# Kernel optimization log

Measured on AMD Instinct MI355X. Metric: run time of the kernel, lower is better.

Reference implementation:

```python
import jax, jax.numpy as jnp
import numpy as np

N_CELLS = 50000
DEG = 32
NNZ = N_CELLS * DEG
D_IN = 64
D_OUT = 64
NEG_SLOPE = 0.2


def setup_inputs() -> dict:
    key = jax.random.key(0)
    k0, k1, k2, k3, k4 = jax.random.split(key, 5)
    x_source = jax.random.normal(k0, (N_CELLS, D_IN), jnp.float32)
    # COO indices of the sparse neighborhood matrix N: DEG entries per row
    edge_rows = jnp.repeat(jnp.arange(N_CELLS, dtype=jnp.int32), DEG)
    edge_cols = jax.random.randint(k1, (NNZ,), 0, N_CELLS, dtype=jnp.int32)
    neighborhood_values = jax.random.uniform(k2, (NNZ,), jnp.float32)
    # xavier_uniform-ish scales (exact init irrelevant for correctness baseline)
    W0 = jax.random.normal(k3, (D_IN, D_OUT), jnp.float32) * (1.414 / np.sqrt(D_IN))
    a0 = jax.random.normal(k4, (2 * D_OUT, 1), jnp.float32) * 0.1
    return {
        "x_source": x_source,
        "edge_rows": edge_rows,
        "edge_cols": edge_cols,
        "neighborhood_values": neighborhood_values,
        "W0": W0,
        "a0": a0,
    }


def reference(x_source, edge_rows, edge_cols, neighborhood_values, W0, a0):
    # message = X W_p  : [n_cells, d_out]
    message = x_source @ W0
    d = message.shape[1]
    # [X_i || X_j] a  ==  (X_i a_src) + (X_j a_dst); compute node-level dot first,
    # then gather per edge (avoids materializing [nnz, 2d] concat)
    a_src = a0[:d, 0]
    a_dst = a0[d:, 0]
    node_src = message @ a_src  # [n_cells]
    node_dst = message @ a_dst  # [n_cells]
    e = jax.nn.leaky_relu(node_src[edge_rows] + node_dst[edge_cols],
                          negative_slope=NEG_SLOPE)  # [nnz]
    # sparse_row_norm: divide each edge value by its row sum (softmax=False path)
    row_sum = jax.ops.segment_sum(e, edge_rows, num_segments=N_CELLS)
    att = e / row_sum[edge_rows]
    # Hadamard product N^1 \odot A_1, then SpMM with message
    vals = neighborhood_values * att  # [nnz]
    out = jax.ops.segment_sum(vals[:, None] * message[edge_cols], edge_rows,
                              num_segments=N_CELLS)  # [n_cells, d_out]
    # update_func='relu'
    return jax.nn.relu(out)
```

## Files before the change

kernel.cpp:

```cpp
#include <hip/hip_runtime.h>
#include <hip/hip_fp16.h>

#define N_CELLS 50000
#define DEG 32
#define DIM 64
#define NEG_SLOPE 0.2

__global__ __launch_bounds__(256)
void gat_prep(const float* __restrict__ x,
              const float* __restrict__ W0,
              const float* __restrict__ a0,
              __half* __restrict__ x2,
              double* __restrict__ ns,
              double* __restrict__ nd) {
  __shared__ double2 p_s[DIM];

  const int tid = threadIdx.x;
  if (tid < DIM) {
    double ps = 0.0, pd = 0.0;
    const float4* w4 = (const float4*)(W0 + tid * DIM);
#pragma unroll
    for (int q = 0; q < DIM / 4; ++q) {
      float4 w = w4[q];
      ps = fma((double)w.x, (double)a0[4 * q + 0], ps);
      ps = fma((double)w.y, (double)a0[4 * q + 1], ps);
      ps = fma((double)w.z, (double)a0[4 * q + 2], ps);
      ps = fma((double)w.w, (double)a0[4 * q + 3], ps);
      pd = fma((double)w.x, (double)a0[DIM + 4 * q + 0], pd);
      pd = fma((double)w.y, (double)a0[DIM + 4 * q + 1], pd);
      pd = fma((double)w.z, (double)a0[DIM + 4 * q + 2], pd);
      pd = fma((double)w.w, (double)a0[DIM + 4 * q + 3], pd);
    }
    p_s[tid] = make_double2(ps, pd);
  }
  __syncthreads();

  const int gtid = blockIdx.x * 256 + tid;
  const int nthreads = gridDim.x * 256;

  const float2* xf2 = (const float2*)x;
  __half2* xh2 = (__half2*)x2;
  for (int i = gtid; i < N_CELLS * DIM / 2; i += nthreads) {
    float2 v = xf2[i];
    xh2[i] = __float22half2_rn(v);
  }

  for (int r = gtid; r < N_CELLS; r += nthreads) {
    const float4* x4 = (const float4*)(x + (size_t)r * DIM);
    double s0 = 0.0, s1 = 0.0, d0 = 0.0, d1 = 0.0;
#pragma unroll
    for (int q = 0; q < DIM / 4; ++q) {
      float4 v = x4[q];
      double2 p0 = p_s[4 * q + 0], p1 = p_s[4 * q + 1];
      double2 p2 = p_s[4 * q + 2], p3 = p_s[4 * q + 3];
      s0 = fma((double)v.x, p0.x, s0); d0 = fma((double)v.x, p0.y, d0);
      s1 = fma((double)v.y, p1.x, s1); d1 = fma((double)v.y, p1.y, d1);
      s0 = fma((double)v.z, p2.x, s0); d0 = fma((double)v.z, p2.y, d0);
      s1 = fma((double)v.w, p3.x, s1); d1 = fma((double)v.w, p3.y, d1);
    }
    ns[r] = s0 + s1;
    nd[r] = d0 + d1;
  }
}

__global__ __launch_bounds__(256)
void gat_edges(const __half* __restrict__ x2,
               const int* __restrict__ ecol,
               const float* __restrict__ nv,
               const float* __restrict__ W0,
               const double* __restrict__ ns,
               const double* __restrict__ nd,
               float* __restrict__ out) {
  __shared__ __align__(16) float w_s[4][2][DEG];
  __shared__ __align__(16) int c_s[4][2][DEG];
  __shared__ __align__(16) float h_s[4][2][DIM];

  const int lane = threadIdx.x & 63;
  const int wid = threadIdx.x >> 6;
  const int half = lane >> 5;
  const int sub = lane & 31;

  float w0c[DIM];
#pragma unroll
  for (int k = 0; k < DIM; ++k) w0c[k] = W0[k * DIM + lane];

  const int gwave = blockIdx.x * 4 + wid;
  const int nwaves = gridDim.x * 4;
  const int npairs = N_CELLS / 2;

  for (int p = gwave; p < npairs; p += nwaves) {
    const int r0 = 2 * p;
    const int myrow = r0 + half;

    const int eidx = r0 * DEG + lane;
    const int col = ecol[eidx];
    const float nvv = nv[eidx];
    double z = ns[myrow] + nd[col];
    double e = (z >= 0.0) ? z : NEG_SLOPE * z;
    double rs = e;
#pragma unroll
    for (int m = 16; m >= 1; m >>= 1) rs += __shfl_xor(rs, m, 64);
    w_s[wid][half][sub] = (float)((double)nvv * (e / rs));
    c_s[wid][half][sub] = col;

    const unsigned* xp = (const unsigned*)x2;
    float ax = 0.0f, ay = 0.0f;
#pragma unroll
    for (int j = 0; j < DEG; ++j) {
      int c = c_s[wid][half][j];
      float w = w_s[wid][half][j];
      unsigned pk = xp[(size_t)c * (DIM / 2) + sub];
      float2 xv = __half22float2(*(const __half2*)&pk);
      ax = fmaf(w, xv.x, ax);
      ay = fmaf(w, xv.y, ay);
    }
    ((float2*)h_s[wid][half])[sub] = make_float2(ax, ay);

    float oA = 0.0f, oB = 0.0f;
    const float4* hA = (const float4*)h_s[wid][0];
    const float4* hB = (const float4*)h_s[wid][1];
#pragma unroll
    for (int q = 0; q < DIM / 4; ++q) {
      float4 a = hA[q];
      float4 b = hB[q];
      oA = fmaf(a.x, w0c[4 * q + 0], oA); oB = fmaf(b.x, w0c[4 * q + 0], oB);
      oA = fmaf(a.y, w0c[4 * q + 1], oA); oB = fmaf(b.y, w0c[4 * q + 1], oB);
      oA = fmaf(a.z, w0c[4 * q + 2], oA); oB = fmaf(b.z, w0c[4 * q + 2], oB);
      oA = fmaf(a.w, w0c[4 * q + 3], oA); oB = fmaf(b.w, w0c[4 * q + 3], oB);
    }
    out[(size_t)r0 * DIM + lane] = fmaxf(oA, 0.0f);
    out[(size_t)(r0 + 1) * DIM + lane] = fmaxf(oB, 0.0f);
  }
}

extern "C" void kernel_launch(void* const* d_in, const int* in_sizes, int n_in,
                              void* d_out, int out_size, void* d_ws, size_t ws_size,
                              hipStream_t stream) {
  const float* x = (const float*)d_in[0];
  const int* ecol = (const int*)d_in[2];
  const float* nv = (const float*)d_in[3];
  const float* W0 = (const float*)d_in[4];
  const float* a0 = (const float*)d_in[5];
  float* out = (float*)d_out;

  __half* x2 = (__half*)d_ws;
  double* ns = (double*)((char*)d_ws + (size_t)N_CELLS * DIM * sizeof(__half));
  double* nd = ns + N_CELLS;

  hipLaunchKernelGGL(gat_prep, dim3(512), dim3(256), 0, stream,
                     x, W0, a0, x2, ns, nd);
  hipLaunchKernelGGL(gat_edges, dim3(2500), dim3(256), 0, stream,
                     x2, ecol, nv, W0, ns, nd, out);
}
```

Measured before the change: 127.5 us.

## Split gather into two feature-half passes with precomputed fp16 edge weights

Edge attention weights are now computed once by a separate kernel and stored as fp16, and the x fp16 copy is split into two 32-wide feature halves. The gather/projection runs in two passes, each touching only half the features so the gathered working set (3.2 MB per half) fits in cache better. The first pass writes a partial output and the second adds it and applies relu. The cost is two extra kernel launches, re-reading the column indices, an extra partial-output round trip, and fp16 rounding of the weights.

```diff
diff --git a/kernel.cpp b/kernel.cpp
--- a/kernel.cpp
+++ b/kernel.cpp
@@ -4,13 +4,16 @@
 #define N_CELLS 50000
 #define DEG 32
 #define DIM 64
+#define HALF_DIM 32
 #define NEG_SLOPE 0.2
+#define NPAIRS (N_CELLS / 2)
 
 __global__ __launch_bounds__(256)
 void gat_prep(const float* __restrict__ x,
               const float* __restrict__ W0,
               const float* __restrict__ a0,
-              __half* __restrict__ x2,
+              __half* __restrict__ xA,
+              __half* __restrict__ xB,
               double* __restrict__ ns,
               double* __restrict__ nd) {
   __shared__ double2 p_s[DIM];
@@ -35,92 +38,117 @@
   }
   __syncthreads();
 
-  const int gtid = blockIdx.x * 256 + tid;
-  const int nthreads = gridDim.x * 256;
-
-  const float2* xf2 = (const float2*)x;
-  __half2* xh2 = (__half2*)x2;
-  for (int i = gtid; i < N_CELLS * DIM / 2; i += nthreads) {
-    float2 v = xf2[i];
-    xh2[i] = __float22half2_rn(v);
+  const int r = blockIdx.x * 256 + tid;
+  if (r >= N_CELLS) return;
+
+  const float4* x4 = (const float4*)(x + (size_t)r * DIM);
+  double s0 = 0.0, s1 = 0.0, d0 = 0.0, d1 = 0.0;
+  __half2 hbuf[DIM / 2];
+#pragma unroll
+  for (int q = 0; q < DIM / 4; ++q) {
+    float4 v = x4[q];
+    double2 p0 = p_s[4 * q + 0], p1 = p_s[4 * q + 1];
+    double2 p2 = p_s[4 * q + 2], p3 = p_s[4 * q + 3];
+    s0 = fma((double)v.x, p0.x, s0); d0 = fma((double)v.x, p0.y, d0);
+    s1 = fma((double)v.y, p1.x, s1); d1 = fma((double)v.y, p1.y, d1);
+    s0 = fma((double)v.z, p2.x, s0); d0 = fma((double)v.z, p2.y, d0);
+    s1 = fma((double)v.w, p3.x, s1); d1 = fma((double)v.w, p3.y, d1);
+    hbuf[2 * q + 0] = __float22half2_rn(make_float2(v.x, v.y));
+    hbuf[2 * q + 1] = __float22half2_rn(make_float2(v.z, v.w));
   }
-
-  for (int r = gtid; r < N_CELLS; r += nthreads) {
-    const float4* x4 = (const float4*)(x + (size_t)r * DIM);
-    double s0 = 0.0, s1 = 0.0, d0 = 0.0, d1 = 0.0;
-#pragma unroll
-    for (int q = 0; q < DIM / 4; ++q) {
-      float4 v = x4[q];
-      double2 p0 = p_s[4 * q + 0], p1 = p_s[4 * q + 1];
-      double2 p2 = p_s[4 * q + 2], p3 = p_s[4 * q + 3];
-      s0 = fma((double)v.x, p0.x, s0); d0 = fma((double)v.x, p0.y, d0);
-      s1 = fma((double)v.y, p1.x, s1); d1 = fma((double)v.y, p1.y, d1);
-      s0 = fma((double)v.z, p2.x, s0); d0 = fma((double)v.z, p2.y, d0);
-      s1 = fma((double)v.w, p3.x, s1); d1 = fma((double)v.w, p3.y, d1);
-    }
-    ns[r] = s0 + s1;
-    nd[r] = d0 + d1;
-  }
+  ns[r] = s0 + s1;
+  nd[r] = d0 + d1;
+
+  const uint4* src = (const uint4*)hbuf;
+  uint4* pA = (uint4*)(xA + (size_t)r * HALF_DIM);
+  uint4* pB = (uint4*)(xB + (size_t)r * HALF_DIM);
+#pragma unroll
+  for (int i = 0; i < 4; ++i) pA[i] = src[i];
+#pragma unroll
+  for (int i = 0; i < 4; ++i) pB[i] = src[4 + i];
 }
 
 __global__ __launch_bounds__(256)
-void gat_edges(const __half* __restrict__ x2,
-               const int* __restrict__ ecol,
-               const float* __restrict__ nv,
-               const float* __restrict__ W0,
-               const double* __restrict__ ns,
-               const double* __restrict__ nd,
-               float* __restrict__ out) {
-  __shared__ __align__(16) float w_s[4][2][DEG];
-  __shared__ __align__(16) int c_s[4][2][DEG];
-  __shared__ __align__(16) float h_s[4][2][DIM];
+void gat_w(const int* __restrict__ ecol,
+           const float* __restrict__ nv,
+           const double* __restrict__ ns,
+           const double* __restrict__ nd,
+           unsigned short* __restrict__ w16) {
+  const int lane = threadIdx.x & 63;
+  const int wid = threadIdx.x >> 6;
+  const int p = blockIdx.x * 4 + wid;
+  if (p >= NPAIRS) return;
+
+  const int r0 = 2 * p;
+  const int half = lane >> 5;
+  const int eidx = r0 * DEG + lane;
+
+  const int col = __builtin_nontemporal_load(ecol + eidx);
+  const float nvv = __builtin_nontemporal_load(nv + eidx);
+  double z = ns[r0 + half] + nd[col];
+  double e = (z >= 0.0) ? z : NEG_SLOPE * z;
+  double rs = e;
+#pragma unroll
+  for (int m = 16; m >= 1; m >>= 1) rs += __shfl_xor(rs, m, 64);
+  const float w = (float)((double)nvv * (e / rs));
+  const __half hw = __float2half(w);
+  __builtin_nontemporal_store(*(const unsigned short*)&hw, w16 + eidx);
+}
+
+template <int PASS>
+__global__ __launch_bounds__(256)
+void gat_pass(const __half* __restrict__ xH,
+              const int* __restrict__ ecol,
+              const unsigned short* __restrict__ w16,
+              const float* __restrict__ W0,
+              float* __restrict__ outp,
+              float* __restrict__ out) {
+  __shared__ __align__(16) float h_s[4][2][HALF_DIM];
 
   const int lane = threadIdx.x & 63;
   const int wid = threadIdx.x >> 6;
   const int half = lane >> 5;
   const int sub = lane & 31;
-
-  float w0c[DIM];
-#pragma unroll
-  for (int k = 0; k < DIM; ++k) w0c[k] = W0[k * DIM + lane];
+  const int par = sub >> 4;
+  const int d = sub & 15;
+
+  float w0c[HALF_DIM];
+#pragma unroll
+  for (int k = 0; k < HALF_DIM; ++k)
+    w0c[k] = W0[(k + HALF_DIM * PASS) * DIM + lane];
 
   const int gwave = blockIdx.x * 4 + wid;
   const int nwaves = gridDim.x * 4;
-  const int npairs = N_CELLS / 2;
-
-  for (int p = gwave; p < npairs; p += nwaves) {
+  const unsigned* xp = (const unsigned*)xH;
+
+  for (int p = gwave; p < NPAIRS; p += nwaves) {
     const int r0 = 2 * p;
-    const int myrow = r0 + half;
-
     const int eidx = r0 * DEG + lane;
-    const int col = ecol[eidx];
-    const float nvv = nv[eidx];
-    double z = ns[myrow] + nd[col];
-    double e = (z >= 0.0) ? z : NEG_SLOPE * z;
-    double rs = e;
-#pragma unroll
-    for (int m = 16; m >= 1; m >>= 1) rs += __shfl_xor(rs, m, 64);
-    w_s[wid][half][sub] = (float)((double)nvv * (e / rs));
-    c_s[wid][half][sub] = col;
-
-    const unsigned* xp = (const unsigned*)x2;
-    float ax = 0.0f, ay = 0.0f;
-#pragma unroll
-    for (int j = 0; j < DEG; ++j) {
-      int c = c_s[wid][half][j];
-      float w = w_s[wid][half][j];
-      unsigned pk = xp[(size_t)c * (DIM / 2) + sub];
+    const int col = __builtin_nontemporal_load(ecol + eidx);
+    const unsigned short uw = __builtin_nontemporal_load(w16 + eidx);
+    const float wv = __half2float(*(const __half*)&uw);
+
+    float a0f = 0.0f, a1f = 0.0f;
+#pragma unroll
+    for (int q = 0; q < 16; ++q) {
+      const int j = 2 * q + par;
+      const int src = (half << 5) | j;
+      const int c = __shfl(col, src, 64);
+      const float w = __shfl(wv, src, 64);
+      unsigned pk = xp[(size_t)c * (HALF_DIM / 2) + d];
       float2 xv = __half22float2(*(const __half2*)&pk);
-      ax = fmaf(w, xv.x, ax);
-      ay = fmaf(w, xv.y, ay);
-    }
-    ((float2*)h_s[wid][half])[sub] = make_float2(ax, ay);
+      a0f = fmaf(w, xv.x, a0f);
+      a1f = fmaf(w, xv.y, a1f);
+    }
+    a0f += __shfl_xor(a0f, 16, 64);
+    a1f += __shfl_xor(a1f, 16, 64);
+    if (par == 0) ((float2*)h_s[wid][half])[d] = make_float2(a0f, a1f);
 
     float oA = 0.0f, oB = 0.0f;
     const float4* hA = (const float4*)h_s[wid][0];
     const float4* hB = (const float4*)h_s[wid][1];
 #pragma unroll
-    for (int q = 0; q < DIM / 4; ++q) {
+    for (int q = 0; q < HALF_DIM / 4; ++q) {
       float4 a = hA[q];
       float4 b = hB[q];
       oA = fmaf(a.x, w0c[4 * q + 0], oA); oB = fmaf(b.x, w0c[4 * q + 0], oB);
@@ -128,8 +156,18 @@
       oA = fmaf(a.z, w0c[4 * q + 2], oA); oB = fmaf(b.z, w0c[4 * q + 2], oB);
       oA = fmaf(a.w, w0c[4 * q + 3], oA); oB = fmaf(b.w, w0c[4 * q + 3], oB);
     }
-    out[(size_t)r0 * DIM + lane] = fmaxf(oA, 0.0f);
-    out[(size_t)(r0 + 1) * DIM + lane] = fmaxf(oB, 0.0f);
+
+    const size_t oidx0 = (size_t)r0 * DIM + lane;
+    const size_t oidx1 = (size_t)(r0 + 1) * DIM + lane;
+    if (PASS == 0) {
+      __builtin_nontemporal_store(oA, outp + oidx0);
+      __builtin_nontemporal_store(oB, outp + oidx1);
+    } else {
+      const float pA = __builtin_nontemporal_load(outp + oidx0);
+      const float pB = __builtin_nontemporal_load(outp + oidx1);
+      __builtin_nontemporal_store(fmaxf(pA + oA, 0.0f), out + oidx0);
+      __builtin_nontemporal_store(fmaxf(pB + oB, 0.0f), out + oidx1);
+    }
   }
 }
 
@@ -143,12 +181,20 @@
   const float* a0 = (const float*)d_in[5];
   float* out = (float*)d_out;
 
-  __half* x2 = (__half*)d_ws;
-  double* ns = (double*)((char*)d_ws + (size_t)N_CELLS * DIM * sizeof(__half));
+  char* wsb = (char*)d_ws;
+  __half* xA = (__half*)wsb;
+  __half* xB = (__half*)(wsb + (size_t)N_CELLS * HALF_DIM * 2);
+  unsigned short* w16 = (unsigned short*)(wsb + (size_t)2 * N_CELLS * HALF_DIM * 2);
+  double* ns = (double*)(wsb + (size_t)2 * N_CELLS * HALF_DIM * 2 + (size_t)N_CELLS * DEG * 2);
   double* nd = ns + N_CELLS;
-
-  hipLaunchKernelGGL(gat_prep, dim3(512), dim3(256), 0, stream,
-                     x, W0, a0, x2, ns, nd);
-  hipLaunchKernelGGL(gat_edges, dim3(2500), dim3(256), 0, stream,
-                     x2, ecol, nv, W0, ns, nd, out);
-}
+  float* outp = (float*)(nd + N_CELLS);
+
+  hipLaunchKernelGGL(gat_prep, dim3((N_CELLS + 255) / 256), dim3(256), 0, stream,
+                     x, W0, a0, xA, xB, ns, nd);
+  hipLaunchKernelGGL(gat_w, dim3((NPAIRS + 3) / 4), dim3(256), 0, stream,
+                     ecol, nv, ns, nd, w16);
+  hipLaunchKernelGGL((gat_pass<0>), dim3(2500), dim3(256), 0, stream,
+                     xA, ecol, w16, W0, outp, out);
+  hipLaunchKernelGGL((gat_pass<1>), dim3(2500), dim3(256), 0, stream,
+                     xB, ecol, w16, W0, outp, out);
+}
```

After: 139.8 us. 9.6% more time.
